# Optimization experiments

Measured on AMD Instinct MI355X. Metric: run time of the kernel, lower is better.

Reference implementation:

```python
import jax, jax.numpy as jnp
import numpy as np
import math

B, T, D, H = 4, 1024, 1024, 16
DK = D // H
TAU_THRESH = 0.3


def setup_inputs() -> dict:
    key = jax.random.key(0)
    ks = jax.random.split(key, 13)
    s = 1.0 / math.sqrt(D)
    return {
        "x": jax.random.normal(ks[0], (B, T, D), dtype=jnp.float32),
        "Wq": jax.random.normal(ks[1], (D, D), dtype=jnp.float32) * s,
        "bq": jax.random.normal(ks[2], (D,), dtype=jnp.float32) * s,
        "Wk": jax.random.normal(ks[3], (D, D), dtype=jnp.float32) * s,
        "bk": jax.random.normal(ks[4], (D,), dtype=jnp.float32) * s,
        "Wv": jax.random.normal(ks[5], (D, D), dtype=jnp.float32) * s,
        "bv": jax.random.normal(ks[6], (D,), dtype=jnp.float32) * s,
        "Wo": jax.random.normal(ks[7], (D, D), dtype=jnp.float32) * s,
        "bo": jax.random.normal(ks[8], (D,), dtype=jnp.float32) * s,
        "Wg1": jax.random.normal(ks[9], (1, D), dtype=jnp.float32) * s,
        "bg1": jax.random.normal(ks[10], (1,), dtype=jnp.float32) * s,
        "Wg2": jax.random.normal(ks[11], (1, D), dtype=jnp.float32) * s,
        "bg2": jax.random.normal(ks[12], (1,), dtype=jnp.float32) * s,
    }


def reference(x, Wq, bq, Wk, bk, Wv, bv, Wo, bo, Wg1, bg1, Wg2, bg2):
    b, t, d = x.shape
    # projections (torch Linear: y = x @ W.T + b)
    Q = (x @ Wq.T + bq).reshape(b, t, H, DK).transpose(0, 2, 1, 3)  # [B,H,T,dk]
    K = (x @ Wk.T + bk).reshape(b, t, H, DK).transpose(0, 2, 1, 3)
    V = (x @ Wv.T + bv).reshape(b, t, H, DK).transpose(0, 2, 1, 3)
    scores = jnp.einsum("bhqd,bhkd->bhqk", Q, K) / math.sqrt(DK)  # [B,H,T,T]
    # confidence gates from first-token query context [B, H*dk] = [B, D]
    context = Q[:, :, 0, :].reshape(b, d)
    q1 = jax.nn.sigmoid(context @ Wg1.T + bg1)  # [B,1]
    q2 = jax.nn.sigmoid(context @ Wg2.T + bg2)  # [B,1]
    c = jnp.clip(q1 * q2, 1e-8, 1.0)            # [B,1]
    tau = jnp.where(c < TAU_THRESH, 1.0 / c, jnp.ones_like(c)).reshape(b, 1, 1, 1)
    p = jax.nn.softmax(scores / tau, axis=-1)
    cb = c.reshape(b, 1, 1, 1)
    p_gated = cb * p + (1.0 - cb) * (1.0 / t)
    u = jnp.mean(1.0 - c, axis=-1, keepdims=True)  # [B,1]
    attn_out = jnp.einsum("bhqk,bhkd->bhqd", p_gated, V)
    attn_out = attn_out.transpose(0, 2, 1, 3).reshape(b, t, d)
    output = attn_out @ Wo.T + bo
    return output, u
```

## Files before the change

kernel.cpp:

```cpp
#include <hip/hip_runtime.h>
#include <stdint.h>

typedef short bf16x8 __attribute__((ext_vector_type(8)));
typedef float f32x4 __attribute__((ext_vector_type(4)));

#define MFMA_BF16(a, b, c) __builtin_amdgcn_mfma_f32_16x16x32_bf16((a), (b), (c), 0, 0, 0)

__device__ __forceinline__ short f2bf(float x) {
  union { float f; uint32_t u; } v; v.f = x;
  uint32_t r = (v.u + 0x7FFFu + ((v.u >> 16) & 1u)) >> 16;
  return (short)r;
}
__device__ __forceinline__ uint32_t rnd_bf_hi(float x) {
  union { float f; uint32_t u; } v; v.f = x;
  return v.u + 0x7FFFu + ((v.u >> 16) & 1u);
}
__device__ __forceinline__ uint32_t pack2bf(float a, float b) {
  return __builtin_amdgcn_perm(rnd_bf_hi(b), rnd_bf_hi(a), 0x07060302);
}
__device__ __forceinline__ float fexp2(float x) {
#if __has_builtin(__builtin_amdgcn_exp2f)
  return __builtin_amdgcn_exp2f(x);
#else
  return __expf(x * 0.6931471805599453f);
#endif
}
__device__ __forceinline__ void async16(const void* g, void* l) {
  __builtin_amdgcn_global_load_lds(
      (const __attribute__((address_space(1))) uint32_t*)g,
      (__attribute__((address_space(3))) uint32_t*)l, 16, 0, 0);
}

__global__ __launch_bounds__(256) void prep_k(
    const float* __restrict__ x, const float* __restrict__ Wq,
    const float* __restrict__ Wk, const float* __restrict__ Wv,
    const float* __restrict__ Wo, const float* __restrict__ bq,
    short* __restrict__ xb, short* __restrict__ Wqb, short* __restrict__ Wkb,
    short* __restrict__ Wvb, short* __restrict__ Wob, float* __restrict__ ctx) {
  __shared__ float xs[1024];
  const int bid = blockIdx.x;
  const int tid = threadIdx.x;
  if (bid < 8192) {
    const float* src; short* dst; int idx;
    if (bid < 4096) {
      src = x; dst = xb; idx = (bid << 8) + tid;
    } else {
      const int r = bid - 4096;
      const int z = r >> 10;
      src = (z == 0) ? Wq : (z == 1) ? Wk : (z == 2) ? Wv : Wo;
      dst = (z == 0) ? Wqb : (z == 1) ? Wkb : (z == 2) ? Wvb : Wob;
      idx = ((r & 1023) << 8) + tid;
    }
    float4 v = ((const float4*)src)[idx];
    short4 o;
    o.x = f2bf(v.x); o.y = f2bf(v.y); o.z = f2bf(v.z); o.w = f2bf(v.w);
    ((short4*)dst)[idx] = o;
  } else {
    const int r = bid - 8192;
    const int b = r >> 4;
    const int n0 = (r & 15) << 6;
    for (int i = tid; i < 1024; i += 256) xs[i] = x[b * 1048576 + i];
    __syncthreads();
    const int w = tid >> 6, lane = tid & 63;
    const float4* xv4 = (const float4*)xs;
    for (int rr = 0; rr < 16; ++rr) {
      const int n = n0 + (w << 4) + rr;
      const float4* wrow = (const float4*)(Wq + n * 1024);
      float p = 0.f;
#pragma unroll
      for (int c2 = 0; c2 < 4; ++c2) {
        float4 wv = wrow[lane + (c2 << 6)];
        float4 xv = xv4[lane + (c2 << 6)];
        p += xv.x * wv.x + xv.y * wv.y + xv.z * wv.z + xv.w * wv.w;
      }
#pragma unroll
      for (int off = 32; off; off >>= 1) p += __shfl_xor(p, off);
      if (lane == 0) ctx[b * 1024 + n] = p + bq[n];
    }
  }
}

template <bool SWP>
__device__ __forceinline__ void qkv_core128(
    const short* __restrict__ A, const short* __restrict__ W,
    const float* __restrict__ bias, short* __restrict__ out,
    short* As, short* Bs, int m0, int n0) {
  const int tid = threadIdx.x;
  const int w = tid >> 6, lane = tid & 63;
  const int m15 = lane & 15, quad = lane >> 4;
  const int wr = w >> 1, wc = w & 1;

  f32x4 acc[4][4];
#pragma unroll
  for (int i = 0; i < 4; ++i)
#pragma unroll
    for (int j = 0; j < 4; ++j) { f32x4 zz = {0.f, 0.f, 0.f, 0.f}; acc[i][j] = zz; }

  const int srow = (w << 5) + (lane >> 2);
  const int sxor = (srow >> 1) & 3;
  const int scol = (((lane & 3) ^ sxor) << 3);
  const short* ga0 = A + (m0 + srow) * 1024 + scol;
  const short* ga1 = ga0 + 16 * 1024;
  const short* gb0 = W + (n0 + srow) * 1024 + scol;
  const short* gb1 = gb0 + 16 * 1024;
  short* la0 = &As[srow * 32 + ((lane & 3) << 3)];
  short* la1 = la0 + 512;
  short* lb0 = &Bs[srow * 32 + ((lane & 3) << 3)];
  short* lb1 = lb0 + 512;

  async16(ga0, la0); async16(ga1, la1);
  async16(gb0, lb0); async16(gb1, lb1);
  __syncthreads();

  for (int kt = 0; kt < 32; ++kt) {
    const int buf = kt & 1;
    if (kt < 31) {
      const int nb = (buf ^ 1) << 12;
      const int off = (kt + 1) << 5;
      async16(ga0 + off, la0 + nb); async16(ga1 + off, la1 + nb);
      async16(gb0 + off, lb0 + nb); async16(gb1 + off, lb1 + nb);
    }
    const short* Ab = As + (buf << 12);
    const short* Bb = Bs + (buf << 12);
    bf16x8 a[4], b[4];
#pragma unroll
    for (int i = 0; i < 4; ++i) {
      const int ra = (wr << 6) + (i << 4) + m15;
      a[i] = *(const bf16x8*)(&Ab[ra * 32 + ((quad ^ ((ra >> 1) & 3)) << 3)]);
    }
#pragma unroll
    for (int j = 0; j < 4; ++j) {
      const int rb = (wc << 6) + (j << 4) + m15;
      b[j] = *(const bf16x8*)(&Bb[rb * 32 + ((quad ^ ((rb >> 1) & 3)) << 3)]);
    }
#pragma unroll
    for (int i = 0; i < 4; ++i)
#pragma unroll
      for (int j = 0; j < 4; ++j) {
        if (SWP) acc[i][j] = MFMA_BF16(b[j], a[i], acc[i][j]);
        else     acc[i][j] = MFMA_BF16(a[i], b[j], acc[i][j]);
      }
    if (kt < 31) __syncthreads();
  }

  if (SWP) {
#pragma unroll
    for (int j = 0; j < 4; ++j) {
      const int n = n0 + (wc << 6) + (j << 4) + (quad << 2);
      const float4 bv = *(const float4*)(bias + n);
      const int hh = n >> 6, dk0 = n & 63;
#pragma unroll
      for (int i = 0; i < 4; ++i) {
        const int m = m0 + (wr << 6) + (i << 4) + m15;
        const int bb = m >> 10, tt = m & 1023;
        uint2 st;
        st.x = pack2bf(acc[i][j][0] + bv.x, acc[i][j][1] + bv.y);
        st.y = pack2bf(acc[i][j][2] + bv.z, acc[i][j][3] + bv.w);
        *(uint2*)(out + (((bb << 4) + hh) << 16) + (tt << 6) + dk0) = st;
      }
    }
  } else {
#pragma unroll
    for (int j = 0; j < 4; ++j) {
      const int n = n0 + (wc << 6) + (j << 4) + m15;
      const float bv = bias[n];
      const int hh = n >> 6, dk = n & 63;
#pragma unroll
      for (int i = 0; i < 4; ++i) {
        const int m = m0 + (wr << 6) + (i << 4) + (quad << 2);
        const int bb = m >> 10, t0 = m & 1023;
        uint2 st;
        st.x = pack2bf(acc[i][j][0] + bv, acc[i][j][1] + bv);
        st.y = pack2bf(acc[i][j][2] + bv, acc[i][j][3] + bv);
        *(uint2*)(out + (((bb << 4) + hh) << 16) + (dk << 10) + t0) = st;
      }
    }
  }
}

__global__ __launch_bounds__(256) void gemm_qkv(
    const short* __restrict__ xb,
    const short* __restrict__ Wqb, const short* __restrict__ Wkb, const short* __restrict__ Wvb,
    const float* __restrict__ bq, const float* __restrict__ bk, const float* __restrict__ bv,
    short* __restrict__ Qh, short* __restrict__ Kh, short* __restrict__ Vt,
    const float* __restrict__ ctx, const float* __restrict__ Wg1,
    const float* __restrict__ bg1, const float* __restrict__ Wg2,
    const float* __restrict__ bg2, float* __restrict__ gates,
    float* __restrict__ u_out) {
  __shared__ short As[8192];
  __shared__ short Bs[8192];
  const int bid = blockIdx.x;
  if (bid < 768) {
    const int z = bid >> 8;
    const int r = bid & 255;
    const int m0 = (r & 31) << 7, n0 = (r >> 5) << 7;
    if (z == 0)      qkv_core128<true >(xb, Wqb, bq, Qh, As, Bs, m0, n0);
    else if (z == 1) qkv_core128<true >(xb, Wkb, bk, Kh, As, Bs, m0, n0);
    else             qkv_core128<false>(xb, Wvb, bv, Vt, As, Bs, m0, n0);
    return;
  }
  float* red = (float*)As;
  const int tid = threadIdx.x, w = tid >> 6, lane = tid & 63;
  for (int b = 0; b < 4; ++b) {
    float4 cv = ((const float4*)(ctx + b * 1024))[tid];
    float4 w1 = ((const float4*)Wg1)[tid];
    float4 w2 = ((const float4*)Wg2)[tid];
    float p1 = cv.x * w1.x + cv.y * w1.y + cv.z * w1.z + cv.w * w1.w;
    float p2 = cv.x * w2.x + cv.y * w2.y + cv.z * w2.z + cv.w * w2.w;
#pragma unroll
    for (int off = 32; off; off >>= 1) { p1 += __shfl_xor(p1, off); p2 += __shfl_xor(p2, off); }
    if (lane == 0) { red[w] = p1; red[8 + w] = p2; }
    __syncthreads();
    if (tid == 0) {
      float g1 = red[0] + red[1] + red[2] + red[3] + bg1[0];
      float g2 = red[8] + red[9] + red[10] + red[11] + bg2[0];
      float q1 = 1.f / (1.f + expf(-g1));
      float q2 = 1.f / (1.f + expf(-g2));
      float c = fminf(fmaxf(q1 * q2, 1e-8f), 1.0f);
      gates[b * 2 + 0] = c;
      gates[b * 2 + 1] = (c < 0.3f ? c : 1.0f) * 0.125f * 1.4426950408889634f;
      u_out[b] = 1.0f - c;
    }
    __syncthreads();
  }
}

__global__ __launch_bounds__(256) void gemm_out(const short* __restrict__ Ab_,
                                                const short* __restrict__ Wo,
                                                const float* __restrict__ bo,
                                                float* __restrict__ Cout) {
  const int m0 = blockIdx.x << 7;
  const int n0 = blockIdx.y << 7;
  const int tid = threadIdx.x;
  const int w = tid >> 6, lane = tid & 63;
  const int m15 = lane & 15, quad = lane >> 4;
  const int wr = w >> 1, wc = w & 1;

  __shared__ short As[8192];
  __shared__ short Bs[8192];

  f32x4 acc[4][4];
#pragma unroll
  for (int i = 0; i < 4; ++i)
#pragma unroll
    for (int j = 0; j < 4; ++j) { f32x4 zz = {0.f, 0.f, 0.f, 0.f}; acc[i][j] = zz; }

  const int srow = (w << 5) + (lane >> 2);
  const int sxor = (srow >> 1) & 3;
  const int scol = (((lane & 3) ^ sxor) << 3);
  const short* ga0 = Ab_ + (m0 + srow) * 1024 + scol;
  const short* ga1 = ga0 + 16 * 1024;
  const short* gb0 = Wo + (n0 + srow) * 1024 + scol;
  const short* gb1 = gb0 + 16 * 1024;
  short* la0 = &As[srow * 32 + ((lane & 3) << 3)];
  short* la1 = la0 + 512;
  short* lb0 = &Bs[srow * 32 + ((lane & 3) << 3)];
  short* lb1 = lb0 + 512;

  async16(ga0, la0); async16(ga1, la1);
  async16(gb0, lb0); async16(gb1, lb1);
  __syncthreads();

  for (int kt = 0; kt < 32; ++kt) {
    const int buf = kt & 1;
    if (kt < 31) {
      const int nb = (buf ^ 1) << 12;
      const int off = (kt + 1) << 5;
      async16(ga0 + off, la0 + nb); async16(ga1 + off, la1 + nb);
      async16(gb0 + off, lb0 + nb); async16(gb1 + off, lb1 + nb);
    }
    const short* Ab = As + (buf << 12);
    const short* Bb = Bs + (buf << 12);
    bf16x8 a[4], b[4];
#pragma unroll
    for (int i = 0; i < 4; ++i) {
      const int ra = (wr << 6) + (i << 4) + m15;
      a[i] = *(const bf16x8*)(&Ab[ra * 32 + ((quad ^ ((ra >> 1) & 3)) << 3)]);
    }
#pragma unroll
    for (int j = 0; j < 4; ++j) {
      const int rb = (wc << 6) + (j << 4) + m15;
      b[j] = *(const bf16x8*)(&Bb[rb * 32 + ((quad ^ ((rb >> 1) & 3)) << 3)]);
    }
#pragma unroll
    for (int i = 0; i < 4; ++i)
#pragma unroll
      for (int j = 0; j < 4; ++j)
        acc[i][j] = MFMA_BF16(a[i], b[j], acc[i][j]);
    if (kt < 31) __syncthreads();
  }

#pragma unroll
  for (int j = 0; j < 4; ++j) {
    const int n = n0 + (wc << 6) + (j << 4) + m15;
    const float bb_ = bo[n];
#pragma unroll
    for (int i = 0; i < 4; ++i) {
      const int mb = m0 + (wr << 6) + (i << 4) + (quad << 2);
#pragma unroll
      for (int r = 0; r < 4; ++r)
        Cout[(mb + r) * 1024 + n] = acc[i][j][r] + bb_;
    }
  }
}

__global__ __launch_bounds__(256, 2) void attn_k(const short* __restrict__ Qh,
                                                 const short* __restrict__ Kh,
                                                 const short* __restrict__ Vt,
                                                 const float* __restrict__ gates,
                                                 short* __restrict__ attnb) {
  const int bh = blockIdx.x;
  const int b = bh >> 4, h = bh & 15;
  const int q0 = blockIdx.y << 7;
  const int tid = threadIdx.x;
  const int w = tid >> 6, lane = tid & 63;
  const int m15 = lane & 15, quad = lane >> 4;

  __shared__ short Ks[2][4096];
  __shared__ short Vs[3][4096];

  const short* ksrc = Kh + bh * 65536;
  const short* vsrc = Vt + bh * 65536;

  const float sl = gates[b * 2 + 1];

  const short* qsrcA = Qh + ((bh << 10) + q0 + (w << 4) + m15) * 64;
  const short* qsrcB = qsrcA + 64 * 64;
  const bf16x8 qA0 = *(const bf16x8*)(qsrcA + (quad << 3));
  const bf16x8 qA1 = *(const bf16x8*)(qsrcA + 32 + (quad << 3));
  const bf16x8 qB0 = *(const bf16x8*)(qsrcB + (quad << 3));
  const bf16x8 qB1 = *(const bf16x8*)(qsrcB + 32 + (quad << 3));

  const bf16x8 vone = {0x3F80, 0x3F80, 0x3F80, 0x3F80, 0x3F80, 0x3F80, 0x3F80, 0x3F80};

  const int off0 = tid, off1 = tid + 256;
  const int r0 = off0 >> 3, cb0 = (off0 & 7) ^ (r0 & 7);
  const int r1 = off1 >> 3, cb1 = (off1 & 7) ^ (r1 & 7);

#define STAGE(kv, kb, vb)                                                      \
  do {                                                                         \
    async16(ksrc + (((kv) << 6) + r0) * 64 + (cb0 << 3), &Ks[kb][off0 << 3]);  \
    async16(ksrc + (((kv) << 6) + r1) * 64 + (cb1 << 3), &Ks[kb][off1 << 3]);  \
    async16(vsrc + r0 * 1024 + ((kv) << 6) + (cb0 << 3), &Vs[vb][off0 << 3]);  \
    async16(vsrc + r1 * 1024 + ((kv) << 6) + (cb1 << 3), &Vs[vb][off1 << 3]);  \
  } while (0)

  STAGE(0, 0, 0);

  float lsumA = 0.f, lsumB = 0.f;
  f32x4 oA[4], oB[4], o_mv[4];
#pragma unroll
  for (int jd = 0; jd < 4; ++jd) {
    f32x4 zz = {0.f, 0.f, 0.f, 0.f};
    oA[jd] = zz; oB[jd] = zz; o_mv[jd] = zz;
  }

  const int srcA = ((quad & 1) << 5) + m15;
  const int srcB = srcA + 16;
  const bool selhi = (quad & 2) != 0;

#define BUILD_PF(pf, pk)                                                       \
  do {                                                                         \
    _Pragma("unroll")                                                          \
    for (int Hh = 0; Hh < 2; ++Hh) {                                           \
      uint32_t f[4];                                                           \
      _Pragma("unroll")                                                        \
      for (int rp = 0; rp < 2; ++rp) {                                         \
        uint32_t alo = (uint32_t)__shfl((int)pk[2 * Hh][rp], srcA);            \
        uint32_t ahi = (uint32_t)__shfl((int)pk[2 * Hh + 1][rp], srcA);        \
        uint32_t blo = (uint32_t)__shfl((int)pk[2 * Hh][rp], srcB);            \
        uint32_t bhi = (uint32_t)__shfl((int)pk[2 * Hh + 1][rp], srcB);        \
        f[rp]     = selhi ? ahi : alo;                                         \
        f[2 + rp] = selhi ? bhi : blo;                                         \
      }                                                                        \
      pf[Hh] = *(bf16x8*)f;                                                    \
    }                                                                          \
  } while (0)

#define PV_STEP(Vb, pfa, pfb)                                                  \
  do {                                                                         \
    _Pragma("unroll")                                                          \
    for (int jd = 0; jd < 4; ++jd) {                                           \
      const int row = (jd << 4) + m15;                                         \
      const int sw = row & 7;                                                  \
      bf16x8 v0 = *(const bf16x8*)((Vb) + (row << 6) + ((quad ^ sw) << 3));    \
      bf16x8 v1 = *(const bf16x8*)((Vb) + (row << 6) + (((quad + 4) ^ sw) << 3)); \
      oA[jd] = MFMA_BF16(v0, pfa[0], oA[jd]);                                  \
      oA[jd] = MFMA_BF16(v1, pfa[1], oA[jd]);                                  \
      oB[jd] = MFMA_BF16(v0, pfb[0], oB[jd]);                                  \
      oB[jd] = MFMA_BF16(v1, pfb[1], oB[jd]);                                  \
      o_mv[jd] = MFMA_BF16(v0, vone, o_mv[jd]);                                \
      o_mv[jd] = MFMA_BF16(v1, vone, o_mv[jd]);                                \
    }                                                                          \
  } while (0)

  bf16x8 pfpA[2], pfpB[2];
  pfpA[0] = (bf16x8){0,0,0,0,0,0,0,0}; pfpA[1] = pfpA[0];
  pfpB[0] = pfpA[0]; pfpB[1] = pfpA[0];

  for (int kv = 0; kv < 16; ++kv) {
    __syncthreads();
    if (kv < 15) STAGE(kv + 1, (kv + 1) & 1, (kv + 1) % 3);
    const short* Kb = &Ks[kv & 1][0];

    f32x4 sA[4], sB[4];
#pragma unroll
    for (int s = 0; s < 4; ++s) {
      const int row = (s << 4) + m15;
      const int sw = row & 7;
      bf16x8 a0 = *(const bf16x8*)(Kb + (row << 6) + ((quad ^ sw) << 3));
      bf16x8 a1 = *(const bf16x8*)(Kb + (row << 6) + (((quad + 4) ^ sw) << 3));
      f32x4 zA = {0.f, 0.f, 0.f, 0.f};
      zA = MFMA_BF16(a0, qA0, zA);
      zA = MFMA_BF16(a1, qA1, zA);
      sA[s] = zA;
      f32x4 zB = {0.f, 0.f, 0.f, 0.f};
      zB = MFMA_BF16(a0, qB0, zB);
      zB = MFMA_BF16(a1, qB1, zB);
      sB[s] = zB;
    }

    if (kv > 0) {
      const short* Vb = &Vs[(kv - 1) % 3][0];
      PV_STEP(Vb, pfpA, pfpB);
    }

    uint32_t pkA[4][2], pkB[4][2];
#pragma unroll
    for (int s = 0; s < 4; ++s) {
      float a0 = fexp2(sA[s][0] * sl);
      float a1 = fexp2(sA[s][1] * sl);
      float a2 = fexp2(sA[s][2] * sl);
      float a3 = fexp2(sA[s][3] * sl);
      lsumA += (a0 + a1) + (a2 + a3);
      pkA[s][0] = pack2bf(a0, a1);
      pkA[s][1] = pack2bf(a2, a3);
      float b0 = fexp2(sB[s][0] * sl);
      float b1 = fexp2(sB[s][1] * sl);
      float b2 = fexp2(sB[s][2] * sl);
      float b3 = fexp2(sB[s][3] * sl);
      lsumB += (b0 + b1) + (b2 + b3);
      pkB[s][0] = pack2bf(b0, b1);
      pkB[s][1] = pack2bf(b2, b3);
    }

    bf16x8 pfA[2], pfB[2];
    BUILD_PF(pfA, pkA);
    BUILD_PF(pfB, pkB);
    pfpA[0] = pfA[0]; pfpA[1] = pfA[1];
    pfpB[0] = pfB[0]; pfpB[1] = pfB[1];
  }

  {
    const short* Vb = &Vs[15 % 3][0];
    PV_STEP(Vb, pfpA, pfpB);
  }
#undef STAGE
#undef BUILD_PF
#undef PV_STEP

  float lA = lsumA;
  lA += __shfl_xor(lA, 16);
  lA += __shfl_xor(lA, 32);
  float lB = lsumB;
  lB += __shfl_xor(lB, 16);
  lB += __shfl_xor(lB, 32);

  const float cg = gates[b * 2 + 0];
  const float sc0A = cg / lA;
  const float sc0B = cg / lB;
  const float coef = (1.0f - cg) * (1.0f / 1024.0f);
  const int qrowA = q0 + (w << 4) + m15;
  short* orowA = attnb + ((b << 10) + qrowA) * 1024 + (h << 6);
  short* orowB = orowA + 64 * 1024;
#pragma unroll
  for (int jd = 0; jd < 4; ++jd) {
    uint2 stA;
    stA.x = pack2bf(sc0A * oA[jd][0] + coef * o_mv[jd][0],
                    sc0A * oA[jd][1] + coef * o_mv[jd][1]);
    stA.y = pack2bf(sc0A * oA[jd][2] + coef * o_mv[jd][2],
                    sc0A * oA[jd][3] + coef * o_mv[jd][3]);
    *(uint2*)(orowA + (jd << 4) + (quad << 2)) = stA;
    uint2 stB;
    stB.x = pack2bf(sc0B * oB[jd][0] + coef * o_mv[jd][0],
                    sc0B * oB[jd][1] + coef * o_mv[jd][1]);
    stB.y = pack2bf(sc0B * oB[jd][2] + coef * o_mv[jd][2],
                    sc0B * oB[jd][3] + coef * o_mv[jd][3]);
    *(uint2*)(orowB + (jd << 4) + (quad << 2)) = stB;
  }
}

extern "C" void kernel_launch(void* const* d_in, const int* in_sizes, int n_in,
                              void* d_out, int out_size, void* d_ws, size_t ws_size,
                              hipStream_t stream) {
  const float* x   = (const float*)d_in[0];
  const float* Wq  = (const float*)d_in[1];
  const float* bq  = (const float*)d_in[2];
  const float* Wk  = (const float*)d_in[3];
  const float* bk  = (const float*)d_in[4];
  const float* Wv  = (const float*)d_in[5];
  const float* bv  = (const float*)d_in[6];
  const float* Wo  = (const float*)d_in[7];
  const float* bo  = (const float*)d_in[8];
  const float* Wg1 = (const float*)d_in[9];
  const float* bg1 = (const float*)d_in[10];
  const float* Wg2 = (const float*)d_in[11];
  const float* bg2 = (const float*)d_in[12];
  float* out = (float*)d_out;

  char* ws = (char*)d_ws;
  short* xb   = (short*)(ws + 0);
  short* Wqb  = (short*)(ws + 8388608);
  short* Wkb  = (short*)(ws + 10485760);
  short* Wvb  = (short*)(ws + 12582912);
  short* Wob  = (short*)(ws + 14680064);
  short* Qh   = (short*)(ws + 16777216);
  short* Kh   = (short*)(ws + 25165824);
  short* Vt   = (short*)(ws + 33554432);
  short* attb = (short*)(ws + 41943040);
  float* ctx  = (float*)(ws + 50331648);
  float* gat  = (float*)(ws + 50348032);

  prep_k<<<8256, 256, 0, stream>>>(x, Wq, Wk, Wv, Wo, bq,
                                   xb, Wqb, Wkb, Wvb, Wob, ctx);
  gemm_qkv<<<769, 256, 0, stream>>>(xb, Wqb, Wkb, Wvb, bq, bk, bv,
                                    Qh, Kh, Vt,
                                    ctx, Wg1, bg1, Wg2, bg2, gat,
                                    out + 4194304);
  attn_k<<<dim3(64, 8), 256, 0, stream>>>(Qh, Kh, Vt, gat, attb);
  gemm_out<<<dim3(32, 8), 256, 0, stream>>>(attb, Wob, bo, out);
}
```

Baseline: 211.6 us.

## Halve per-block tile in attention and output GEMM to raise block count

The attention kernel now handles 64 query rows per block instead of 128, so each wave computes one 16-row query tile instead of two. The grid doubles and launch bounds allow 4 blocks per SM. The output projection GEMM likewise shrinks its M tile from 128 to 64, doubling its grid. More blocks improve occupancy and balance across the many CUs. The cost is lower K/V and weight reuse per block, which means more global and LDS traffic, and the o_mv ones-MFMA is now done once per 16 rows instead of once per 32.

```diff
diff --git a/kernel.cpp b/kernel.cpp
--- a/kernel.cpp
+++ b/kernel.cpp
@@ -229,52 +229,51 @@
                                                 const short* __restrict__ Wo,
                                                 const float* __restrict__ bo,
                                                 float* __restrict__ Cout) {
-  const int m0 = blockIdx.x << 7;
+  const int m0 = blockIdx.x << 6;
   const int n0 = blockIdx.y << 7;
   const int tid = threadIdx.x;
   const int w = tid >> 6, lane = tid & 63;
   const int m15 = lane & 15, quad = lane >> 4;
   const int wr = w >> 1, wc = w & 1;
 
-  __shared__ short As[8192];
+  __shared__ short As[4096];
   __shared__ short Bs[8192];
 
-  f32x4 acc[4][4];
-#pragma unroll
-  for (int i = 0; i < 4; ++i)
+  f32x4 acc[2][4];
+#pragma unroll
+  for (int i = 0; i < 2; ++i)
 #pragma unroll
     for (int j = 0; j < 4; ++j) { f32x4 zz = {0.f, 0.f, 0.f, 0.f}; acc[i][j] = zz; }
 
-  const int srow = (w << 5) + (lane >> 2);
-  const int sxor = (srow >> 1) & 3;
-  const int scol = (((lane & 3) ^ sxor) << 3);
-  const short* ga0 = Ab_ + (m0 + srow) * 1024 + scol;
-  const short* ga1 = ga0 + 16 * 1024;
-  const short* gb0 = Wo + (n0 + srow) * 1024 + scol;
+  const int arow = (w << 4) + (lane >> 2);
+  const int axor = (arow >> 1) & 3;
+  const short* gaA = Ab_ + (m0 + arow) * 1024 + (((lane & 3) ^ axor) << 3);
+  short* laA = &As[arow * 32 + ((lane & 3) << 3)];
+  const int brow = (w << 5) + (lane >> 2);
+  const int bxor = (brow >> 1) & 3;
+  const short* gb0 = Wo + (n0 + brow) * 1024 + (((lane & 3) ^ bxor) << 3);
   const short* gb1 = gb0 + 16 * 1024;
-  short* la0 = &As[srow * 32 + ((lane & 3) << 3)];
-  short* la1 = la0 + 512;
-  short* lb0 = &Bs[srow * 32 + ((lane & 3) << 3)];
+  short* lb0 = &Bs[brow * 32 + ((lane & 3) << 3)];
   short* lb1 = lb0 + 512;
 
-  async16(ga0, la0); async16(ga1, la1);
+  async16(gaA, laA);
   async16(gb0, lb0); async16(gb1, lb1);
   __syncthreads();
 
   for (int kt = 0; kt < 32; ++kt) {
     const int buf = kt & 1;
     if (kt < 31) {
-      const int nb = (buf ^ 1) << 12;
       const int off = (kt + 1) << 5;
-      async16(ga0 + off, la0 + nb); async16(ga1 + off, la1 + nb);
-      async16(gb0 + off, lb0 + nb); async16(gb1 + off, lb1 + nb);
-    }
-    const short* Ab = As + (buf << 12);
+      async16(gaA + off, laA + ((buf ^ 1) << 11));
+      async16(gb0 + off, lb0 + ((buf ^ 1) << 12));
+      async16(gb1 + off, lb1 + ((buf ^ 1) << 12));
+    }
+    const short* Ab = As + (buf << 11);
     const short* Bb = Bs + (buf << 12);
-    bf16x8 a[4], b[4];
-#pragma unroll
-    for (int i = 0; i < 4; ++i) {
-      const int ra = (wr << 6) + (i << 4) + m15;
+    bf16x8 a[2], b[4];
+#pragma unroll
+    for (int i = 0; i < 2; ++i) {
+      const int ra = (wr << 5) + (i << 4) + m15;
       a[i] = *(const bf16x8*)(&Ab[ra * 32 + ((quad ^ ((ra >> 1) & 3)) << 3)]);
     }
 #pragma unroll
@@ -283,7 +282,7 @@
       b[j] = *(const bf16x8*)(&Bb[rb * 32 + ((quad ^ ((rb >> 1) & 3)) << 3)]);
     }
 #pragma unroll
-    for (int i = 0; i < 4; ++i)
+    for (int i = 0; i < 2; ++i)
 #pragma unroll
       for (int j = 0; j < 4; ++j)
         acc[i][j] = MFMA_BF16(a[i], b[j], acc[i][j]);
@@ -295,8 +294,8 @@
     const int n = n0 + (wc << 6) + (j << 4) + m15;
     const float bb_ = bo[n];
 #pragma unroll
-    for (int i = 0; i < 4; ++i) {
-      const int mb = m0 + (wr << 6) + (i << 4) + (quad << 2);
+    for (int i = 0; i < 2; ++i) {
+      const int mb = m0 + (wr << 5) + (i << 4) + (quad << 2);
 #pragma unroll
       for (int r = 0; r < 4; ++r)
         Cout[(mb + r) * 1024 + n] = acc[i][j][r] + bb_;
@@ -304,14 +303,14 @@
   }
 }
 
-__global__ __launch_bounds__(256, 2) void attn_k(const short* __restrict__ Qh,
+__global__ __launch_bounds__(256, 4) void attn_k(const short* __restrict__ Qh,
                                                  const short* __restrict__ Kh,
                                                  const short* __restrict__ Vt,
                                                  const float* __restrict__ gates,
                                                  short* __restrict__ attnb) {
   const int bh = blockIdx.x;
   const int b = bh >> 4, h = bh & 15;
-  const int q0 = blockIdx.y << 7;
+  const int q0 = blockIdx.y << 6;
   const int tid = threadIdx.x;
   const int w = tid >> 6, lane = tid & 63;
   const int m15 = lane & 15, quad = lane >> 4;
@@ -324,12 +323,9 @@
 
   const float sl = gates[b * 2 + 1];
 
-  const short* qsrcA = Qh + ((bh << 10) + q0 + (w << 4) + m15) * 64;
-  const short* qsrcB = qsrcA + 64 * 64;
-  const bf16x8 qA0 = *(const bf16x8*)(qsrcA + (quad << 3));
-  const bf16x8 qA1 = *(const bf16x8*)(qsrcA + 32 + (quad << 3));
-  const bf16x8 qB0 = *(const bf16x8*)(qsrcB + (quad << 3));
-  const bf16x8 qB1 = *(const bf16x8*)(qsrcB + 32 + (quad << 3));
+  const short* qsrc = Qh + ((bh << 10) + q0 + (w << 4) + m15) * 64;
+  const bf16x8 qb0 = *(const bf16x8*)(qsrc + (quad << 3));
+  const bf16x8 qb1 = *(const bf16x8*)(qsrc + 32 + (quad << 3));
 
   const bf16x8 vone = {0x3F80, 0x3F80, 0x3F80, 0x3F80, 0x3F80, 0x3F80, 0x3F80, 0x3F80};
 
@@ -347,12 +343,12 @@
 
   STAGE(0, 0, 0);
 
-  float lsumA = 0.f, lsumB = 0.f;
-  f32x4 oA[4], oB[4], o_mv[4];
+  float lsum = 0.f;
+  f32x4 oA[4], o_mv[4];
 #pragma unroll
   for (int jd = 0; jd < 4; ++jd) {
     f32x4 zz = {0.f, 0.f, 0.f, 0.f};
-    oA[jd] = zz; oB[jd] = zz; o_mv[jd] = zz;
+    oA[jd] = zz; o_mv[jd] = zz;
   }
 
   const int srcA = ((quad & 1) << 5) + m15;
@@ -377,7 +373,7 @@
     }                                                                          \
   } while (0)
 
-#define PV_STEP(Vb, pfa, pfb)                                                  \
+#define PV_STEP(Vb, pfa)                                                       \
   do {                                                                         \
     _Pragma("unroll")                                                          \
     for (int jd = 0; jd < 4; ++jd) {                                           \
@@ -387,106 +383,80 @@
       bf16x8 v1 = *(const bf16x8*)((Vb) + (row << 6) + (((quad + 4) ^ sw) << 3)); \
       oA[jd] = MFMA_BF16(v0, pfa[0], oA[jd]);                                  \
       oA[jd] = MFMA_BF16(v1, pfa[1], oA[jd]);                                  \
-      oB[jd] = MFMA_BF16(v0, pfb[0], oB[jd]);                                  \
-      oB[jd] = MFMA_BF16(v1, pfb[1], oB[jd]);                                  \
       o_mv[jd] = MFMA_BF16(v0, vone, o_mv[jd]);                                \
       o_mv[jd] = MFMA_BF16(v1, vone, o_mv[jd]);                                \
     }                                                                          \
   } while (0)
 
-  bf16x8 pfpA[2], pfpB[2];
-  pfpA[0] = (bf16x8){0,0,0,0,0,0,0,0}; pfpA[1] = pfpA[0];
-  pfpB[0] = pfpA[0]; pfpB[1] = pfpA[0];
+  bf16x8 pfp[2];
+  pfp[0] = (bf16x8){0, 0, 0, 0, 0, 0, 0, 0};
+  pfp[1] = pfp[0];
 
   for (int kv = 0; kv < 16; ++kv) {
     __syncthreads();
     if (kv < 15) STAGE(kv + 1, (kv + 1) & 1, (kv + 1) % 3);
     const short* Kb = &Ks[kv & 1][0];
 
-    f32x4 sA[4], sB[4];
+    f32x4 sA[4];
 #pragma unroll
     for (int s = 0; s < 4; ++s) {
       const int row = (s << 4) + m15;
       const int sw = row & 7;
       bf16x8 a0 = *(const bf16x8*)(Kb + (row << 6) + ((quad ^ sw) << 3));
       bf16x8 a1 = *(const bf16x8*)(Kb + (row << 6) + (((quad + 4) ^ sw) << 3));
-      f32x4 zA = {0.f, 0.f, 0.f, 0.f};
-      zA = MFMA_BF16(a0, qA0, zA);
-      zA = MFMA_BF16(a1, qA1, zA);
-      sA[s] = zA;
-      f32x4 zB = {0.f, 0.f, 0.f, 0.f};
-      zB = MFMA_BF16(a0, qB0, zB);
-      zB = MFMA_BF16(a1, qB1, zB);
-      sB[s] = zB;
+      f32x4 zz = {0.f, 0.f, 0.f, 0.f};
+      zz = MFMA_BF16(a0, qb0, zz);
+      zz = MFMA_BF16(a1, qb1, zz);
+      sA[s] = zz;
     }
 
     if (kv > 0) {
       const short* Vb = &Vs[(kv - 1) % 3][0];
-      PV_STEP(Vb, pfpA, pfpB);
-    }
-
-    uint32_t pkA[4][2], pkB[4][2];
+      PV_STEP(Vb, pfp);
+    }
+
+    uint32_t pk[4][2];
 #pragma unroll
     for (int s = 0; s < 4; ++s) {
-      float a0 = fexp2(sA[s][0] * sl);
-      float a1 = fexp2(sA[s][1] * sl);
-      float a2 = fexp2(sA[s][2] * sl);
-      float a3 = fexp2(sA[s][3] * sl);
-      lsumA += (a0 + a1) + (a2 + a3);
-      pkA[s][0] = pack2bf(a0, a1);
-      pkA[s][1] = pack2bf(a2, a3);
-      float b0 = fexp2(sB[s][0] * sl);
-      float b1 = fexp2(sB[s][1] * sl);
-      float b2 = fexp2(sB[s][2] * sl);
-      float b3 = fexp2(sB[s][3] * sl);
-      lsumB += (b0 + b1) + (b2 + b3);
-      pkB[s][0] = pack2bf(b0, b1);
-      pkB[s][1] = pack2bf(b2, b3);
-    }
-
-    bf16x8 pfA[2], pfB[2];
-    BUILD_PF(pfA, pkA);
-    BUILD_PF(pfB, pkB);
-    pfpA[0] = pfA[0]; pfpA[1] = pfA[1];
-    pfpB[0] = pfB[0]; pfpB[1] = pfB[1];
+      float p0 = fexp2(sA[s][0] * sl);
+      float p1 = fexp2(sA[s][1] * sl);
+      float p2 = fexp2(sA[s][2] * sl);
+      float p3 = fexp2(sA[s][3] * sl);
+      lsum += (p0 + p1) + (p2 + p3);
+      pk[s][0] = pack2bf(p0, p1);
+      pk[s][1] = pack2bf(p2, p3);
+    }
+
+    bf16x8 pf[2];
+    BUILD_PF(pf, pk);
+    pfp[0] = pf[0]; pfp[1] = pf[1];
   }
 
   {
     const short* Vb = &Vs[15 % 3][0];
-    PV_STEP(Vb, pfpA, pfpB);
+    PV_STEP(Vb, pfp);
   }
 #undef STAGE
 #undef BUILD_PF
 #undef PV_STEP
 
-  float lA = lsumA;
-  lA += __shfl_xor(lA, 16);
-  lA += __shfl_xor(lA, 32);
-  float lB = lsumB;
-  lB += __shfl_xor(lB, 16);
-  lB += __shfl_xor(lB, 32);
+  float l = lsum;
+  l += __shfl_xor(l, 16);
+  l += __shfl_xor(l, 32);
 
   const float cg = gates[b * 2 + 0];
-  const float sc0A = cg / lA;
-  const float sc0B = cg / lB;
+  const float sc0 = cg / l;
   const float coef = (1.0f - cg) * (1.0f / 1024.0f);
-  const int qrowA = q0 + (w << 4) + m15;
-  short* orowA = attnb + ((b << 10) + qrowA) * 1024 + (h << 6);
-  short* orowB = orowA + 64 * 1024;
+  const int qrow = q0 + (w << 4) + m15;
+  short* orow = attnb + ((b << 10) + qrow) * 1024 + (h << 6);
 #pragma unroll
   for (int jd = 0; jd < 4; ++jd) {
-    uint2 stA;
-    stA.x = pack2bf(sc0A * oA[jd][0] + coef * o_mv[jd][0],
-                    sc0A * oA[jd][1] + coef * o_mv[jd][1]);
-    stA.y = pack2bf(sc0A * oA[jd][2] + coef * o_mv[jd][2],
-                    sc0A * oA[jd][3] + coef * o_mv[jd][3]);
-    *(uint2*)(orowA + (jd << 4) + (quad << 2)) = stA;
-    uint2 stB;
-    stB.x = pack2bf(sc0B * oB[jd][0] + coef * o_mv[jd][0],
-                    sc0B * oB[jd][1] + coef * o_mv[jd][1]);
-    stB.y = pack2bf(sc0B * oB[jd][2] + coef * o_mv[jd][2],
-                    sc0B * oB[jd][3] + coef * o_mv[jd][3]);
-    *(uint2*)(orowB + (jd << 4) + (quad << 2)) = stB;
+    uint2 st;
+    st.x = pack2bf(sc0 * oA[jd][0] + coef * o_mv[jd][0],
+                   sc0 * oA[jd][1] + coef * o_mv[jd][1]);
+    st.y = pack2bf(sc0 * oA[jd][2] + coef * o_mv[jd][2],
+                   sc0 * oA[jd][3] + coef * o_mv[jd][3]);
+    *(uint2*)(orow + (jd << 4) + (quad << 2)) = st;
   }
 }
 
@@ -527,6 +497,6 @@
                                     Qh, Kh, Vt,
                                     ctx, Wg1, bg1, Wg2, bg2, gat,
                                     out + 4194304);
-  attn_k<<<dim3(64, 8), 256, 0, stream>>>(Qh, Kh, Vt, gat, attb);
-  gemm_out<<<dim3(32, 8), 256, 0, stream>>>(attb, Wob, bo, out);
-}
+  attn_k<<<dim3(64, 16), 256, 0, stream>>>(Qh, Kh, Vt, gat, attb);
+  gemm_out<<<dim3(64, 8), 256, 0, stream>>>(attb, Wob, bo, out);
+}
```

After: 206.4 us (median of 2 runs). -2.5%, faster.
